# Performance work log

Measured on AMD Instinct MI355X. Metric: run time of the kernel, lower is better.

Reference implementation:

```python
import jax, jax.numpy as jnp
import numpy as np

N, E = 50000, 640000
DIN, DH, DOUT = 128, 256, 128


def _glorot(k, i, o):
    return jax.random.normal(k, (i, o), jnp.float32) / np.sqrt(i)


def setup_inputs() -> dict:
    key = jax.random.key(0)
    ks = jax.random.split(key, 12)
    return {
        "x": jax.random.normal(ks[0], (N, DIN), jnp.float32),
        "edge_index": jax.random.randint(ks[1], (2, E), 0, N, dtype=jnp.int32),
        # SAGEConv 1: in -> hidden (lin_l on aggregated w/ bias, lin_r on root)
        "W1l": _glorot(ks[2], DIN, DH), "b1l": jnp.zeros((DH,), jnp.float32), "W1r": _glorot(ks[3], DIN, DH),
        "g1": jnp.ones((DH,), jnp.float32), "be1": jnp.zeros((DH,), jnp.float32),
        # skip projection (in != hidden)
        "Wsk": _glorot(ks[4], DIN, DH), "bsk": jnp.zeros((DH,), jnp.float32),
        # SAGEConv 2: hidden -> hidden
        "W2l": _glorot(ks[5], DH, DH), "b2l": jnp.zeros((DH,), jnp.float32), "W2r": _glorot(ks[6], DH, DH),
        "g2": jnp.ones((DH,), jnp.float32), "be2": jnp.zeros((DH,), jnp.float32),
        # SAGEConv 3: hidden -> out
        "W3l": _glorot(ks[7], DH, DOUT), "b3l": jnp.zeros((DOUT,), jnp.float32), "W3r": _glorot(ks[8], DH, DOUT),
    }


def _sage_conv(x, src, dst, Wl, bl, Wr, n):
    # mean aggregation of source features into destination nodes
    msg = x[src]                                                 # [E, d]
    agg = jax.ops.segment_sum(msg, dst, num_segments=n)          # [N, d]
    cnt = jax.ops.segment_sum(jnp.ones((src.shape[0],), x.dtype), dst, num_segments=n)
    agg = agg / jnp.maximum(cnt, 1.0)[:, None]
    return agg @ Wl + bl + x @ Wr


def _layernorm(x, g, b):
    mu = jnp.mean(x, axis=-1, keepdims=True)
    var = jnp.mean((x - mu) ** 2, axis=-1, keepdims=True)
    return (x - mu) * jax.lax.rsqrt(var + 1e-5) * g + b


def reference(x, edge_index, W1l, b1l, W1r, g1, be1, Wsk, bsk,
              W2l, b2l, W2r, g2, be2, W3l, b3l, W3r):
    src, dst = edge_index[0], edge_index[1]
    n = x.shape[0]
    # layer 0: conv -> LN -> relu -> (dropout p=0, eval) -> skip via projection
    h = _sage_conv(x, src, dst, W1l, b1l, W1r, n)
    h = jax.nn.relu(_layernorm(h, g1, be1))
    h = h + (x @ Wsk + bsk)
    # layer 1: conv -> LN -> relu -> residual add (shapes match)
    h2 = _sage_conv(h, src, dst, W2l, b2l, W2r, n)
    h2 = jax.nn.relu(_layernorm(h2, g2, be2)) + h
    # final conv (no norm/act)
    return _sage_conv(h2, src, dst, W3l, b3l, W3r, n)
```

## Files before the change

kernel.cpp:

```cpp
#include <hip/hip_runtime.h>


typedef float floatx4 __attribute__((ext_vector_type(4)));
typedef float floatx2 __attribute__((ext_vector_type(2)));
typedef short bf16x8 __attribute__((ext_vector_type(8)));

__device__ inline unsigned short f2bf(float f) {
    unsigned u = __float_as_uint(f);
    unsigned r = (u + 0x7fffu + ((u >> 16) & 1u)) >> 16;
    return (unsigned short)r;
}
__device__ inline float bf2f_lo(unsigned v) { return __uint_as_float(v << 16); }
__device__ inline float bf2f_hi(unsigned v) { return __uint_as_float(v & 0xffff0000u); }

__device__ inline void gl_lds16(const void* g, void* l) {
    __builtin_amdgcn_global_load_lds((const __attribute__((address_space(1))) unsigned int*)g,
                                     (__attribute__((address_space(3))) unsigned int*)l,
                                     16, 0, 0);
}

__global__ void hist_kernel(const int* __restrict__ dst, int* __restrict__ cnt, int E) {
    int i = blockIdx.x * blockDim.x + threadIdx.x;
    if (i < E) atomicAdd(&cnt[dst[i]], 1);
}

#define SCAN_CHUNK 2048

__global__ __launch_bounds__(256) void scan_blocksums(const int* __restrict__ cnt,
                                                      int* __restrict__ bsum, int N) {
    __shared__ int sh[256];
    int t = threadIdx.x;
    int base = blockIdx.x * SCAN_CHUNK + t * 8;
    int s = 0;
#pragma unroll
    for (int i = 0; i < 8; i++) {
        int idx = base + i;
        if (idx < N) s += cnt[idx];
    }
    sh[t] = s;
    __syncthreads();
    for (int off = 1; off < 256; off <<= 1) {
        int v = (t >= off) ? sh[t - off] : 0;
        __syncthreads();
        sh[t] += v;
        __syncthreads();
    }
    if (t == 255) bsum[blockIdx.x] = sh[255];
}

__global__ __launch_bounds__(256) void scan_bsums(const int* __restrict__ bsum,
                                                  int* __restrict__ boff, int NB,
                                                  int* __restrict__ rowptr, int N, int E) {
    __shared__ int sh[256];
    int t = threadIdx.x;
    int v = (t < NB) ? bsum[t] : 0;
    sh[t] = v;
    __syncthreads();
    for (int off = 1; off < 256; off <<= 1) {
        int u = (t >= off) ? sh[t - off] : 0;
        __syncthreads();
        sh[t] += u;
        __syncthreads();
    }
    if (t < NB) boff[t] = sh[t] - v;
    if (t == 0) rowptr[N] = E;
}

__global__ __launch_bounds__(256) void scan_final(const int* __restrict__ cnt,
                                                  const int* __restrict__ boff,
                                                  int* __restrict__ rowptr,
                                                  int* __restrict__ cursor,
                                                  float* __restrict__ invdeg, int N) {
    __shared__ int sh[256];
    int t = threadIdx.x;
    int base = blockIdx.x * SCAN_CHUNK + t * 8;
    int c[8];
    int s = 0;
#pragma unroll
    for (int i = 0; i < 8; i++) {
        int idx = base + i;
        c[i] = (idx < N) ? cnt[idx] : 0;
        s += c[i];
    }
    sh[t] = s;
    __syncthreads();
    for (int off = 1; off < 256; off <<= 1) {
        int v = (t >= off) ? sh[t - off] : 0;
        __syncthreads();
        sh[t] += v;
        __syncthreads();
    }
    int run = boff[blockIdx.x] + sh[t] - s;
#pragma unroll
    for (int i = 0; i < 8; i++) {
        int idx = base + i;
        if (idx < N) {
            rowptr[idx] = run;
            cursor[idx] = run;
            invdeg[idx] = 1.0f / (float)(c[i] > 1 ? c[i] : 1);
            run += c[i];
        }
    }
}

__global__ void scatter_kernel(const int* __restrict__ src, const int* __restrict__ dst,
                               int* __restrict__ cursor, int* __restrict__ col, int E) {
    int i = blockIdx.x * blockDim.x + threadIdx.x;
    if (i < E) {
        int p = atomicAdd(&cursor[dst[i]], 1);
        col[p] = src[i];
    }
}

__global__ void prep_weights(const float* __restrict__ W1l, const float* __restrict__ W1r,
                             const float* __restrict__ Wsk, const float* __restrict__ W2l,
                             const float* __restrict__ W2r, const float* __restrict__ W3l,
                             const float* __restrict__ W3r, const float* __restrict__ b1l,
                             const float* __restrict__ bsk,
                             unsigned short* __restrict__ WtC, unsigned short* __restrict__ Wt2,
                             unsigned short* __restrict__ Wt3, float* __restrict__ biasC) {
    int i = blockIdx.x * blockDim.x + threadIdx.x;
    if (i < 32768) {
        int k = i >> 8, n = i & 255;
        WtC[n * 256 + k] = f2bf(W1l[i]);
    } else if (i < 65536) {
        int j = i - 32768, k = j >> 8, n = j & 255;
        WtC[n * 256 + 128 + k] = f2bf(W1r[j]);
    } else if (i < 98304) {
        int j = i - 65536, k = j >> 8, n = j & 255;
        WtC[(256 + n) * 256 + 128 + k] = f2bf(Wsk[j]);
    } else if (i < 131072) {
        int j = i - 98304, k = j >> 8, n = j & 255;
        WtC[(256 + n) * 256 + k] = 0;
    } else if (i < 196608) {
        int j = i - 131072, k = j >> 8, n = j & 255;
        Wt2[n * 512 + k] = f2bf(W2l[j]);
    } else if (i < 262144) {
        int j = i - 196608, k = j >> 8, n = j & 255;
        Wt2[n * 512 + 256 + k] = f2bf(W2r[j]);
    } else if (i < 294912) {
        int j = i - 262144, k = j >> 7, n = j & 127;
        Wt3[n * 256 + k] = f2bf(W3l[j]);
    } else if (i < 327680) {
        int j = i - 294912, k = j >> 7, n = j & 127;
        Wt3[(128 + n) * 256 + k] = f2bf(W3r[j]);
    } else if (i < 328192) {
        int j = i - 327680;
        biasC[j] = (j < 256) ? b1l[j] : bsk[j - 256];
    }
}

__global__ void cvt_x2(const float* __restrict__ x, unsigned short* __restrict__ A1cat,
                       unsigned char* __restrict__ X8, int total32) {
    int i = blockIdx.x * blockDim.x + threadIdx.x;
    if (i >= total32) return;
    int r = i >> 5, c4 = (i & 31) * 4;
    float4 v = *(const float4*)(x + (size_t)r * 128 + c4);
    ushort4 o;
    o.x = f2bf(v.x); o.y = f2bf(v.y); o.z = f2bf(v.z); o.w = f2bf(v.w);
    *(ushort4*)(A1cat + (size_t)r * 256 + 128 + c4) = o;
    unsigned wpk = 0;
    wpk = __builtin_amdgcn_cvt_pk_fp8_f32(v.x, v.y, wpk, false);
    wpk = __builtin_amdgcn_cvt_pk_fp8_f32(v.z, v.w, wpk, true);
    *(unsigned*)(X8 + (size_t)r * 128 + c4) = wpk;
}

__device__ inline void acc16_fp8(uint4 v, float m, floatx2* a) {
    floatx2 mm = {m, m};
    floatx2 p;
    p = __builtin_amdgcn_cvt_pk_f32_fp8(v.x, false); a[0] = p * mm + a[0];
    p = __builtin_amdgcn_cvt_pk_f32_fp8(v.x, true);  a[1] = p * mm + a[1];
    p = __builtin_amdgcn_cvt_pk_f32_fp8(v.y, false); a[2] = p * mm + a[2];
    p = __builtin_amdgcn_cvt_pk_f32_fp8(v.y, true);  a[3] = p * mm + a[3];
    p = __builtin_amdgcn_cvt_pk_f32_fp8(v.z, false); a[4] = p * mm + a[4];
    p = __builtin_amdgcn_cvt_pk_f32_fp8(v.z, true);  a[5] = p * mm + a[5];
    p = __builtin_amdgcn_cvt_pk_f32_fp8(v.w, false); a[6] = p * mm + a[6];
    p = __builtin_amdgcn_cvt_pk_f32_fp8(v.w, true);  a[7] = p * mm + a[7];
}

template <int RSB>
__global__ __launch_bounds__(256) void agg_fp8_g(const int* __restrict__ rowptr,
                                                 const int* __restrict__ col,
                                                 const float* __restrict__ invdeg,
                                                 const unsigned char* __restrict__ T8,
                                                 unsigned short* __restrict__ out, int ostride, int N) {
    constexpr int LPR = RSB / 16;
    constexpr int NPW = 64 / LPR;
    int wid = (blockIdx.x * blockDim.x + threadIdx.x) >> 6;
    int lane = threadIdx.x & 63;
    int sub = lane & (LPR - 1);
    int g = lane / LPR;
    int node = wid * NPW + g;
    bool vn = node < N;
    int nc = vn ? node : N - 1;
    int s = rowptr[nc];
    int e = vn ? rowptr[nc + 1] : s;
    const unsigned char* To = T8 + sub * 16;
    floatx2 a[8];
#pragma unroll
    for (int i = 0; i < 8; i++) a[i] = (floatx2){0.f, 0.f};
    for (int j = s; j < e; j += 4) {
        int j1 = (j + 1 < e) ? j + 1 : j;
        int j2 = (j + 2 < e) ? j + 2 : j;
        int j3 = (j + 3 < e) ? j + 3 : j;
        float m1 = (j + 1 < e) ? 1.f : 0.f;
        float m2 = (j + 2 < e) ? 1.f : 0.f;
        float m3 = (j + 3 < e) ? 1.f : 0.f;
        int c0 = col[j], c1 = col[j1], c2 = col[j2], c3 = col[j3];
        uint4 v0 = *(const uint4*)(To + (size_t)c0 * RSB);
        uint4 v1 = *(const uint4*)(To + (size_t)c1 * RSB);
        uint4 v2 = *(const uint4*)(To + (size_t)c2 * RSB);
        uint4 v3 = *(const uint4*)(To + (size_t)c3 * RSB);
        acc16_fp8(v0, 1.f, a);
        acc16_fp8(v1, m1, a);
        acc16_fp8(v2, m2, a);
        acc16_fp8(v3, m3, a);
    }
    if (vn) {
        float inv = invdeg[node];
        uint4 o1, o2;
        o1.x = (unsigned)f2bf(a[0].x * inv) | ((unsigned)f2bf(a[0].y * inv) << 16);
        o1.y = (unsigned)f2bf(a[1].x * inv) | ((unsigned)f2bf(a[1].y * inv) << 16);
        o1.z = (unsigned)f2bf(a[2].x * inv) | ((unsigned)f2bf(a[2].y * inv) << 16);
        o1.w = (unsigned)f2bf(a[3].x * inv) | ((unsigned)f2bf(a[3].y * inv) << 16);
        o2.x = (unsigned)f2bf(a[4].x * inv) | ((unsigned)f2bf(a[4].y * inv) << 16);
        o2.y = (unsigned)f2bf(a[5].x * inv) | ((unsigned)f2bf(a[5].y * inv) << 16);
        o2.z = (unsigned)f2bf(a[6].x * inv) | ((unsigned)f2bf(a[6].y * inv) << 16);
        o2.w = (unsigned)f2bf(a[7].x * inv) | ((unsigned)f2bf(a[7].y * inv) << 16);
        unsigned short* op = out + (size_t)node * ostride + sub * 16;
        *(uint4*)op = o1;
        *(uint4*)(op + 8) = o2;
    }
}

__global__ __launch_bounds__(256) void agg_fin_g(const int* __restrict__ rowptr,
                                                 const int* __restrict__ col,
                                                 const float* __restrict__ invdeg,
                                                 const unsigned short* __restrict__ T,
                                                 const float* __restrict__ R,
                                                 float* __restrict__ out, int N) {
    int wid = (blockIdx.x * blockDim.x + threadIdx.x) >> 6;
    int lane = threadIdx.x & 63;
    int sub = lane & 15;
    int g = lane >> 4;
    int node = wid * 4 + g;
    bool vn = node < N;
    int nc = vn ? node : N - 1;
    int s = rowptr[nc];
    int e = vn ? rowptr[nc + 1] : s;
    const unsigned short* To = T + sub * 8;
    floatx2 a[4];
#pragma unroll
    for (int i = 0; i < 4; i++) a[i] = (floatx2){0.f, 0.f};
    for (int j = s; j < e; j += 4) {
        int j1 = (j + 1 < e) ? j + 1 : j;
        int j2 = (j + 2 < e) ? j + 2 : j;
        int j3 = (j + 3 < e) ? j + 3 : j;
        float m1 = (j + 1 < e) ? 1.f : 0.f;
        float m2 = (j + 2 < e) ? 1.f : 0.f;
        float m3 = (j + 3 < e) ? 1.f : 0.f;
        int c0 = col[j], c1 = col[j1], c2 = col[j2], c3 = col[j3];
        uint4 v0 = *(const uint4*)(To + (size_t)c0 * 128);
        uint4 v1 = *(const uint4*)(To + (size_t)c1 * 128);
        uint4 v2 = *(const uint4*)(To + (size_t)c2 * 128);
        uint4 v3 = *(const uint4*)(To + (size_t)c3 * 128);
        floatx2 mm;
        floatx2 p;
        mm = (floatx2){1.f, 1.f};
        p = (floatx2){bf2f_lo(v0.x), bf2f_hi(v0.x)}; a[0] = p + a[0];
        p = (floatx2){bf2f_lo(v0.y), bf2f_hi(v0.y)}; a[1] = p + a[1];
        p = (floatx2){bf2f_lo(v0.z), bf2f_hi(v0.z)}; a[2] = p + a[2];
        p = (floatx2){bf2f_lo(v0.w), bf2f_hi(v0.w)}; a[3] = p + a[3];
        mm = (floatx2){m1, m1};
        p = (floatx2){bf2f_lo(v1.x), bf2f_hi(v1.x)}; a[0] = p * mm + a[0];
        p = (floatx2){bf2f_lo(v1.y), bf2f_hi(v1.y)}; a[1] = p * mm + a[1];
        p = (floatx2){bf2f_lo(v1.z), bf2f_hi(v1.z)}; a[2] = p * mm + a[2];
        p = (floatx2){bf2f_lo(v1.w), bf2f_hi(v1.w)}; a[3] = p * mm + a[3];
        mm = (floatx2){m2, m2};
        p = (floatx2){bf2f_lo(v2.x), bf2f_hi(v2.x)}; a[0] = p * mm + a[0];
        p = (floatx2){bf2f_lo(v2.y), bf2f_hi(v2.y)}; a[1] = p * mm + a[1];
        p = (floatx2){bf2f_lo(v2.z), bf2f_hi(v2.z)}; a[2] = p * mm + a[2];
        p = (floatx2){bf2f_lo(v2.w), bf2f_hi(v2.w)}; a[3] = p * mm + a[3];
        mm = (floatx2){m3, m3};
        p = (floatx2){bf2f_lo(v3.x), bf2f_hi(v3.x)}; a[0] = p * mm + a[0];
        p = (floatx2){bf2f_lo(v3.y), bf2f_hi(v3.y)}; a[1] = p * mm + a[1];
        p = (floatx2){bf2f_lo(v3.z), bf2f_hi(v3.z)}; a[2] = p * mm + a[2];
        p = (floatx2){bf2f_lo(v3.w), bf2f_hi(v3.w)}; a[3] = p * mm + a[3];
    }
    if (vn) {
        float inv = invdeg[node];
        const float* Rp = R + (size_t)node * 128 + sub * 8;
        float4 r1 = *(const float4*)Rp;
        float4 r2 = *(const float4*)(Rp + 4);
        float4 o1, o2;
        o1.x = a[0].x * inv + r1.x; o1.y = a[0].y * inv + r1.y;
        o1.z = a[1].x * inv + r1.z; o1.w = a[1].y * inv + r1.w;
        o2.x = a[2].x * inv + r2.x; o2.y = a[2].y * inv + r2.y;
        o2.z = a[3].x * inv + r2.z; o2.w = a[3].y * inv + r2.w;
        float* op = out + (size_t)node * 128 + sub * 8;
        *(float4*)op = o1;
        *(float4*)(op + 4) = o2;
    }
}

template <int KIT, int NPAN, int MODE>
__global__ __launch_bounds__(512) void gemm_fused(
    const unsigned short* __restrict__ A, int lda,
    const unsigned short* __restrict__ B, int ldb,
    const float* __restrict__ bias,
    const float* __restrict__ gamma, const float* __restrict__ beta,
    const unsigned short* __restrict__ resid,
    unsigned short* __restrict__ outb,
    unsigned char* __restrict__ h8,
    float* __restrict__ outf, int M) {
    constexpr int COLS = NPAN * 256;
    constexpr int LNW = COLS + 8;
    constexpr int STAGE_E = 128 * 64;
    constexpr int STAGE_F = 2 * STAGE_E / 2;
    constexpr int SMEM_F = (STAGE_F > 32 * LNW) ? STAGE_F : 32 * LNW;
    __shared__ __align__(16) float smemf[SMEM_F];
    unsigned short* sbase = (unsigned short*)smemf;

    int t = threadIdx.x;
    int lane = t & 63, w = t >> 6;
    int bm = blockIdx.x * 128;
    int wm = (w & 1) * 64, wn = (w >> 1) * 64;
    int m16 = lane & 15, kq = lane >> 4;

    floatx4 acc[NPAN][4][4];
#pragma unroll
    for (int p = 0; p < NPAN; p++)
#pragma unroll
        for (int i = 0; i < 4; i++)
#pragma unroll
            for (int j = 0; j < 4; j++) acc[p][i][j] = (floatx4){0.f, 0.f, 0.f, 0.f};

    const int s_row0 = t >> 3;
    const int s_j = t & 7;

    auto stage = [&](int kt, int bsel) {
        unsigned short* s = sbase + bsel * STAGE_E;
        int k0 = kt * 64;
#pragma unroll
        for (int i = 0; i < 2; i++) {
            int row = s_row0 + i * 64;
            int kc = s_j ^ (row & 7);
            int rowA = bm + row;
            if (rowA > M - 1) rowA = M - 1;
            gl_lds16(A + (size_t)rowA * lda + k0 + kc * 8, (void*)&s[(size_t)(i * 512 + t) * 8]);
        }
    };

    stage(0, 0);
    __syncthreads();
    for (int kt = 0; kt < KIT; kt++) {
        if (kt + 1 < KIT) stage(kt + 1, (kt & 1) ^ 1);
        const unsigned short* sA = sbase + (kt & 1) * STAGE_E;
#pragma unroll
        for (int ks = 0; ks < 2; ks++) {
            int kcl = (ks << 2) | kq;
            bf16x8 af[4];
#pragma unroll
            for (int mi = 0; mi < 4; mi++)
                af[mi] = *(const bf16x8*)&sA[(wm + mi * 16 + m16) * 64 + (kcl ^ (m16 & 7)) * 8];
#pragma unroll
            for (int p = 0; p < NPAN; p++) {
                if (MODE == 0 && p == 1 && kt * 64 < 128) continue;
                const unsigned short* Bp = B + (size_t)(wn + p * 256) * ldb + kt * 64;
                bf16x8 bf[4];
#pragma unroll
                for (int ni = 0; ni < 4; ni++)
                    bf[ni] = *(const bf16x8*)&Bp[(size_t)(ni * 16 + m16) * ldb + kcl * 8];
#pragma unroll
                for (int mi = 0; mi < 4; mi++)
#pragma unroll
                    for (int ni = 0; ni < 4; ni++)
                        acc[p][mi][ni] =
                            __builtin_amdgcn_mfma_f32_16x16x32_bf16(af[mi], bf[ni], acc[p][mi][ni], 0, 0, 0);
            }
        }
        __syncthreads();
    }

    float* lnb = smemf;
    int c4 = lane * 4;
    float4 bu = {0.f, 0.f, 0.f, 0.f}, bs = {0.f, 0.f, 0.f, 0.f};
    float4 gv = {0.f, 0.f, 0.f, 0.f}, bv = {0.f, 0.f, 0.f, 0.f};
    float4 b3 = {0.f, 0.f, 0.f, 0.f};
    if (MODE == 0) {
        bu = *(const float4*)&bias[c4];
        bs = *(const float4*)&bias[256 + c4];
        gv = *(const float4*)&gamma[c4];
        bv = *(const float4*)&beta[c4];
    } else if (MODE == 1) {
        bu = *(const float4*)&bias[c4];
        gv = *(const float4*)&gamma[c4];
        bv = *(const float4*)&beta[c4];
    } else {
        if (lane >= 32) b3 = *(const float4*)&bias[c4 - 128];
    }

#pragma unroll
    for (int g4 = 0; g4 < 4; g4++) {
        if (wm == (g4 >> 1) * 64) {
            int mi0 = (g4 & 1) * 2;
#pragma unroll
            for (int p = 0; p < NPAN; p++)
#pragma unroll
                for (int mm = 0; mm < 2; mm++)
#pragma unroll
                    for (int ni = 0; ni < 4; ni++)
#pragma unroll
                        for (int r = 0; r < 4; r++)
                            lnb[(mm * 16 + kq * 4 + r) * LNW + wn + p * 256 + ni * 16 + m16] =
                                acc[p][mi0 + mm][ni][r];
        }
        __syncthreads();
#pragma unroll
        for (int rr = 0; rr < 4; rr++) {
            int lrow = w * 4 + rr;
            int grow = bm + g4 * 32 + lrow;
            bool valid = grow < M;
            float4 u = *(const float4*)&lnb[lrow * LNW + c4];
            if (MODE <= 1) {
                u.x += bu.x; u.y += bu.y; u.z += bu.z; u.w += bu.w;
                float s1 = (u.x + u.y) + (u.z + u.w);
                float s2 = (u.x * u.x + u.y * u.y) + (u.z * u.z + u.w * u.w);
#pragma unroll
                for (int off = 1; off < 64; off <<= 1) {
                    s1 += __shfl_xor(s1, off, 64);
                    s2 += __shfl_xor(s2, off, 64);
                }
                float mu = s1 * (1.f / 256.f);
                float var = s2 * (1.f / 256.f) - mu * mu;
                float rs = rsqrtf(var + 1e-5f);
                float a0, a1, a2, a3;
                if (MODE == 0) {
                    float4 sv = *(const float4*)&lnb[lrow * LNW + 256 + c4];
                    a0 = sv.x + bs.x; a1 = sv.y + bs.y; a2 = sv.z + bs.z; a3 = sv.w + bs.w;
                } else {
                    int gr = valid ? grow : M - 1;
                    uint2 hv = *(const uint2*)(resid + (size_t)gr * 512 + c4);
                    a0 = bf2f_lo(hv.x); a1 = bf2f_hi(hv.x); a2 = bf2f_lo(hv.y); a3 = bf2f_hi(hv.y);
                }
                float o0 = fmaxf((u.x - mu) * rs * gv.x + bv.x, 0.f) + a0;
                float o1 = fmaxf((u.y - mu) * rs * gv.y + bv.y, 0.f) + a1;
                float o2 = fmaxf((u.z - mu) * rs * gv.z + bv.z, 0.f) + a2;
                float o3 = fmaxf((u.w - mu) * rs * gv.w + bv.w, 0.f) + a3;
                if (valid) {
                    ushort4 o;
                    o.x = f2bf(o0); o.y = f2bf(o1); o.z = f2bf(o2); o.w = f2bf(o3);
                    *(ushort4*)(outb + (size_t)grow * 512 + c4) = o;
                    if (MODE == 0) {
                        unsigned wpk = 0;
                        wpk = __builtin_amdgcn_cvt_pk_fp8_f32(o0, o1, wpk, false);
                        wpk = __builtin_amdgcn_cvt_pk_fp8_f32(o2, o3, wpk, true);
                        *(unsigned*)(h8 + (size_t)grow * 256 + c4) = wpk;
                    }
                }
            } else {
                if (valid) {
                    if (lane < 32) {
                        ushort4 o;
                        o.x = f2bf(u.x); o.y = f2bf(u.y); o.z = f2bf(u.z); o.w = f2bf(u.w);
                        *(ushort4*)(outb + (size_t)grow * 128 + c4) = o;
                    } else {
                        float4 o;
                        o.x = u.x + b3.x; o.y = u.y + b3.y; o.z = u.z + b3.z; o.w = u.w + b3.w;
                        *(float4*)(outf + (size_t)grow * 128 + (c4 - 128)) = o;
                    }
                }
            }
        }
        __syncthreads();
    }
}

extern "C" void kernel_launch(void* const* d_in, const int* in_sizes, int n_in,
                              void* d_out, int out_size, void* d_ws, size_t ws_size,
                              hipStream_t stream) {
    const float* x   = (const float*)d_in[0];
    const int*   ei  = (const int*)d_in[1];
    const float* W1l = (const float*)d_in[2];
    const float* b1l = (const float*)d_in[3];
    const float* W1r = (const float*)d_in[4];
    const float* g1  = (const float*)d_in[5];
    const float* be1 = (const float*)d_in[6];
    const float* Wsk = (const float*)d_in[7];
    const float* bsk = (const float*)d_in[8];
    const float* W2l = (const float*)d_in[9];
    const float* b2l = (const float*)d_in[10];
    const float* W2r = (const float*)d_in[11];
    const float* g2  = (const float*)d_in[12];
    const float* be2 = (const float*)d_in[13];
    const float* W3l = (const float*)d_in[14];
    const float* b3l = (const float*)d_in[15];
    const float* W3r = (const float*)d_in[16];

    const int N = in_sizes[0] / 128;
    const int E = in_sizes[1] / 2;
    const int* src = ei;
    const int* dst = ei + E;

    char* p = (char*)d_ws;
    auto alloc = [&](size_t bytes) {
        void* r = (void*)p;
        p += (bytes + 255) & ~(size_t)255;
        return r;
    };
    int*   cnt    = (int*)alloc(sizeof(int) * N);
    int*   rowptr = (int*)alloc(sizeof(int) * (N + 1));
    int*   cursor = (int*)alloc(sizeof(int) * N);
    float* invdeg = (float*)alloc(sizeof(float) * N);
    int*   col    = (int*)alloc(sizeof(int) * E);
    int*   bsum   = (int*)alloc(sizeof(int) * 256);
    int*   boff   = (int*)alloc(sizeof(int) * 256);
    unsigned short* A1cat = (unsigned short*)alloc(sizeof(short) * (size_t)N * 256);
    unsigned short* A2cat = (unsigned short*)alloc(sizeof(short) * (size_t)N * 512);
    float* r3 = (float*)alloc(sizeof(float) * (size_t)N * 128);
    unsigned char* H8 = (unsigned char*)alloc((size_t)N * 256);
    unsigned char* X8 = (unsigned char*)alloc((size_t)N * 128);
    unsigned short* WtC = (unsigned short*)alloc(sizeof(short) * 512 * 256);
    unsigned short* Wt2 = (unsigned short*)alloc(sizeof(short) * 256 * 512);
    unsigned short* Wt3 = (unsigned short*)alloc(sizeof(short) * 256 * 256);
    float* biasC = (float*)alloc(sizeof(float) * 512);
    unsigned short* t3 = A1cat;

    hipMemsetAsync(cnt, 0, sizeof(int) * N, stream);
    hist_kernel<<<(E + 255) / 256, 256, 0, stream>>>(dst, cnt, E);
    int NB = (N + SCAN_CHUNK - 1) / SCAN_CHUNK;
    scan_blocksums<<<NB, 256, 0, stream>>>(cnt, bsum, N);
    scan_bsums<<<1, 256, 0, stream>>>(bsum, boff, NB, rowptr, N, E);
    scan_final<<<NB, 256, 0, stream>>>(cnt, boff, rowptr, cursor, invdeg, N);
    scatter_kernel<<<(E + 255) / 256, 256, 0, stream>>>(src, dst, cursor, col, E);

    prep_weights<<<(328192 + 255) / 256, 256, 0, stream>>>(W1l, W1r, Wsk, W2l, W2r, W3l, W3r,
                                                           b1l, bsk, WtC, Wt2, Wt3, biasC);
    cvt_x2<<<((N * 32) + 255) / 256, 256, 0, stream>>>(x, A1cat, X8, N * 32);

    int mBlocks = (N + 127) / 128;
    int agg1Blocks = (N + 31) / 32;
    int agg2Blocks = (N + 15) / 16;
    int aggFBlocks = (N + 15) / 16;

    agg_fp8_g<128><<<agg1Blocks, 256, 0, stream>>>(rowptr, col, invdeg, X8, A1cat, 256, N);
    gemm_fused<4, 2, 0><<<mBlocks, 512, 0, stream>>>(A1cat, 256, WtC, 256, biasC, g1, be1,
                                                     nullptr, A2cat + 256, H8, nullptr, N);

    agg_fp8_g<256><<<agg2Blocks, 256, 0, stream>>>(rowptr, col, invdeg, H8, A2cat, 512, N);
    gemm_fused<8, 1, 1><<<mBlocks, 512, 0, stream>>>(A2cat, 512, Wt2, 512, b2l, g2, be2,
                                                     A2cat + 256, A2cat, nullptr, nullptr, N);

    gemm_fused<4, 1, 2><<<mBlocks, 512, 0, stream>>>(A2cat, 512, Wt3, 256, b3l, nullptr, nullptr,
                                                     nullptr, t3, nullptr, r3, N);
    agg_fin_g<<<aggFBlocks, 256, 0, stream>>>(rowptr, col, invdeg, t3, r3, (float*)d_out, N);
}
```

Baseline: 376.9 us.

## Fuse layer-2 GEMM+LayerNorm with layer-3 GEMM, keeping h2 in LDS

Layer 2's GEMM with LayerNorm, ReLU and residual is merged with layer 3's dual projection GEMM in one kernel. The bf16 h2 tile is written into shared memory in the swizzled A layout and used directly as the A operand for the second GEMM. This removes one launch plus the global write and re-read of h2. In exchange, shared memory per block grows to about 64KB plus the LayerNorm buffer, which may lower occupancy. The layer-1 GEMM is split out into its own non-templated kernel.

```diff
diff --git a/kernel.cpp b/kernel.cpp
--- a/kernel.cpp
+++ b/kernel.cpp
@@ -266,7 +266,6 @@
         uint4 v3 = *(const uint4*)(To + (size_t)c3 * 128);
         floatx2 mm;
         floatx2 p;
-        mm = (floatx2){1.f, 1.f};
         p = (floatx2){bf2f_lo(v0.x), bf2f_hi(v0.x)}; a[0] = p + a[0];
         p = (floatx2){bf2f_lo(v0.y), bf2f_hi(v0.y)}; a[1] = p + a[1];
         p = (floatx2){bf2f_lo(v0.z), bf2f_hi(v0.z)}; a[2] = p + a[2];
@@ -303,16 +302,15 @@
     }
 }
 
-template <int KIT, int NPAN, int MODE>
-__global__ __launch_bounds__(512) void gemm_fused(
+__global__ __launch_bounds__(512) void gemm_l1(
     const unsigned short* __restrict__ A, int lda,
     const unsigned short* __restrict__ B, int ldb,
     const float* __restrict__ bias,
     const float* __restrict__ gamma, const float* __restrict__ beta,
-    const unsigned short* __restrict__ resid,
     unsigned short* __restrict__ outb,
-    unsigned char* __restrict__ h8,
-    float* __restrict__ outf, int M) {
+    unsigned char* __restrict__ h8, int M) {
+    constexpr int KIT = 4;
+    constexpr int NPAN = 2;
     constexpr int COLS = NPAN * 256;
     constexpr int LNW = COLS + 8;
     constexpr int STAGE_E = 128 * 64;
@@ -326,6 +324,7 @@
     int bm = blockIdx.x * 128;
     int wm = (w & 1) * 64, wn = (w >> 1) * 64;
     int m16 = lane & 15, kq = lane >> 4;
+    const int fsw = m16 & 7;
 
     floatx4 acc[NPAN][4][4];
 #pragma unroll
@@ -337,7 +336,6 @@
 
     const int s_row0 = t >> 3;
     const int s_j = t & 7;
-
     auto stage = [&](int kt, int bsel) {
         unsigned short* s = sbase + bsel * STAGE_E;
         int k0 = kt * 64;
@@ -362,10 +360,10 @@
             bf16x8 af[4];
 #pragma unroll
             for (int mi = 0; mi < 4; mi++)
-                af[mi] = *(const bf16x8*)&sA[(wm + mi * 16 + m16) * 64 + (kcl ^ (m16 & 7)) * 8];
+                af[mi] = *(const bf16x8*)&sA[(wm + mi * 16 + m16) * 64 + (kcl ^ fsw) * 8];
 #pragma unroll
             for (int p = 0; p < NPAN; p++) {
-                if (MODE == 0 && p == 1 && kt * 64 < 128) continue;
+                if (p == 1 && kt * 64 < 128) continue;
                 const unsigned short* Bp = B + (size_t)(wn + p * 256) * ldb + kt * 64;
                 bf16x8 bf[4];
 #pragma unroll
@@ -384,21 +382,10 @@
 
     float* lnb = smemf;
     int c4 = lane * 4;
-    float4 bu = {0.f, 0.f, 0.f, 0.f}, bs = {0.f, 0.f, 0.f, 0.f};
-    float4 gv = {0.f, 0.f, 0.f, 0.f}, bv = {0.f, 0.f, 0.f, 0.f};
-    float4 b3 = {0.f, 0.f, 0.f, 0.f};
-    if (MODE == 0) {
-        bu = *(const float4*)&bias[c4];
-        bs = *(const float4*)&bias[256 + c4];
-        gv = *(const float4*)&gamma[c4];
-        bv = *(const float4*)&beta[c4];
-    } else if (MODE == 1) {
-        bu = *(const float4*)&bias[c4];
-        gv = *(const float4*)&gamma[c4];
-        bv = *(const float4*)&beta[c4];
-    } else {
-        if (lane >= 32) b3 = *(const float4*)&bias[c4 - 128];
-    }
+    float4 bu = *(const float4*)&bias[c4];
+    float4 bs = *(const float4*)&bias[256 + c4];
+    float4 gv = *(const float4*)&gamma[c4];
+    float4 bv = *(const float4*)&beta[c4];
 
 #pragma unroll
     for (int g4 = 0; g4 < 4; g4++) {
@@ -422,53 +409,225 @@
             int grow = bm + g4 * 32 + lrow;
             bool valid = grow < M;
             float4 u = *(const float4*)&lnb[lrow * LNW + c4];
-            if (MODE <= 1) {
-                u.x += bu.x; u.y += bu.y; u.z += bu.z; u.w += bu.w;
-                float s1 = (u.x + u.y) + (u.z + u.w);
-                float s2 = (u.x * u.x + u.y * u.y) + (u.z * u.z + u.w * u.w);
-#pragma unroll
-                for (int off = 1; off < 64; off <<= 1) {
-                    s1 += __shfl_xor(s1, off, 64);
-                    s2 += __shfl_xor(s2, off, 64);
-                }
-                float mu = s1 * (1.f / 256.f);
-                float var = s2 * (1.f / 256.f) - mu * mu;
-                float rs = rsqrtf(var + 1e-5f);
-                float a0, a1, a2, a3;
-                if (MODE == 0) {
-                    float4 sv = *(const float4*)&lnb[lrow * LNW + 256 + c4];
-                    a0 = sv.x + bs.x; a1 = sv.y + bs.y; a2 = sv.z + bs.z; a3 = sv.w + bs.w;
+            u.x += bu.x; u.y += bu.y; u.z += bu.z; u.w += bu.w;
+            float s1 = (u.x + u.y) + (u.z + u.w);
+            float s2 = (u.x * u.x + u.y * u.y) + (u.z * u.z + u.w * u.w);
+#pragma unroll
+            for (int off = 1; off < 64; off <<= 1) {
+                s1 += __shfl_xor(s1, off, 64);
+                s2 += __shfl_xor(s2, off, 64);
+            }
+            float mu = s1 * (1.f / 256.f);
+            float var = s2 * (1.f / 256.f) - mu * mu;
+            float rs = rsqrtf(var + 1e-5f);
+            float4 sv = *(const float4*)&lnb[lrow * LNW + 256 + c4];
+            float a0 = sv.x + bs.x, a1 = sv.y + bs.y, a2 = sv.z + bs.z, a3 = sv.w + bs.w;
+            float o0 = fmaxf((u.x - mu) * rs * gv.x + bv.x, 0.f) + a0;
+            float o1 = fmaxf((u.y - mu) * rs * gv.y + bv.y, 0.f) + a1;
+            float o2 = fmaxf((u.z - mu) * rs * gv.z + bv.z, 0.f) + a2;
+            float o3 = fmaxf((u.w - mu) * rs * gv.w + bv.w, 0.f) + a3;
+            if (valid) {
+                ushort4 o;
+                o.x = f2bf(o0); o.y = f2bf(o1); o.z = f2bf(o2); o.w = f2bf(o3);
+                *(ushort4*)(outb + (size_t)grow * 512 + c4) = o;
+                unsigned wpk = 0;
+                wpk = __builtin_amdgcn_cvt_pk_fp8_f32(o0, o1, wpk, false);
+                wpk = __builtin_amdgcn_cvt_pk_fp8_f32(o2, o3, wpk, true);
+                *(unsigned*)(h8 + (size_t)grow * 256 + c4) = wpk;
+            }
+        }
+        __syncthreads();
+    }
+}
+
+__global__ __launch_bounds__(512) void gemm23_fused(
+    const unsigned short* __restrict__ A,
+    const unsigned short* __restrict__ B2,
+    const float* __restrict__ b2,
+    const float* __restrict__ g2v, const float* __restrict__ be2v,
+    const unsigned short* __restrict__ resid,
+    const unsigned short* __restrict__ B3,
+    const float* __restrict__ b3,
+    unsigned short* __restrict__ t3,
+    float* __restrict__ r3, int M) {
+    constexpr int KIT = 8;
+    constexpr int LNW = 256 + 8;
+    constexpr int STAGE_E = 128 * 64;
+    __shared__ __align__(16) char smem[65536 + 32 * LNW * 4];
+    unsigned short* Ab = (unsigned short*)smem;
+    float* lnb = (float*)(smem + 65536);
+
+    int t = threadIdx.x;
+    int lane = t & 63, w = t >> 6;
+    int bm = blockIdx.x * 128;
+    int wm = (w & 1) * 64, wn = (w >> 1) * 64;
+    int m16 = lane & 15, kq = lane >> 4;
+    const int fsw = m16 & 7;
+
+    floatx4 acc[4][4];
+#pragma unroll
+    for (int i = 0; i < 4; i++)
+#pragma unroll
+        for (int j = 0; j < 4; j++) acc[i][j] = (floatx4){0.f, 0.f, 0.f, 0.f};
+
+    const int s_row0 = t >> 3;
+    const int s_j = t & 7;
+    auto stage = [&](int kt, int bsel) {
+        unsigned short* s = Ab + bsel * STAGE_E;
+        int k0 = kt * 64;
+#pragma unroll
+        for (int i = 0; i < 2; i++) {
+            int row = s_row0 + i * 64;
+            int kc = s_j ^ (row & 7);
+            int rowA = bm + row;
+            if (rowA > M - 1) rowA = M - 1;
+            gl_lds16(A + (size_t)rowA * 512 + k0 + kc * 8, (void*)&s[(size_t)(i * 512 + t) * 8]);
+        }
+    };
+
+    stage(0, 0);
+    __syncthreads();
+    for (int kt = 0; kt < KIT; kt++) {
+        if (kt + 1 < KIT) stage(kt + 1, (kt & 1) ^ 1);
+        const unsigned short* sA = Ab + (kt & 1) * STAGE_E;
+#pragma unroll
+        for (int ks = 0; ks < 2; ks++) {
+            int kcl = (ks << 2) | kq;
+            bf16x8 af[4];
+#pragma unroll
+            for (int mi = 0; mi < 4; mi++)
+                af[mi] = *(const bf16x8*)&sA[(wm + mi * 16 + m16) * 64 + (kcl ^ fsw) * 8];
+            const unsigned short* Bp = B2 + (size_t)wn * 512 + kt * 64;
+            bf16x8 bf[4];
+#pragma unroll
+            for (int ni = 0; ni < 4; ni++)
+                bf[ni] = *(const bf16x8*)&Bp[(size_t)(ni * 16 + m16) * 512 + kcl * 8];
+#pragma unroll
+            for (int mi = 0; mi < 4; mi++)
+#pragma unroll
+                for (int ni = 0; ni < 4; ni++)
+                    acc[mi][ni] =
+                        __builtin_amdgcn_mfma_f32_16x16x32_bf16(af[mi], bf[ni], acc[mi][ni], 0, 0, 0);
+        }
+        __syncthreads();
+    }
+
+    int c4 = lane * 4;
+    float4 bu = *(const float4*)&b2[c4];
+    float4 gv = *(const float4*)&g2v[c4];
+    float4 bv = *(const float4*)&be2v[c4];
+    const int a_kt = lane >> 4;
+    const int a_ch = (lane >> 1) & 7;
+    const int a_wi = (lane & 1) * 4;
+#pragma unroll
+    for (int g4 = 0; g4 < 4; g4++) {
+        if (wm == (g4 >> 1) * 64) {
+            int mi0 = (g4 & 1) * 2;
+#pragma unroll
+            for (int mm = 0; mm < 2; mm++)
+#pragma unroll
+                for (int ni = 0; ni < 4; ni++)
+#pragma unroll
+                    for (int r = 0; r < 4; r++)
+                        lnb[(mm * 16 + kq * 4 + r) * LNW + wn + ni * 16 + m16] =
+                            acc[mi0 + mm][ni][r];
+        }
+        __syncthreads();
+#pragma unroll
+        for (int rr = 0; rr < 4; rr++) {
+            int lrow = w * 4 + rr;
+            int grow = bm + g4 * 32 + lrow;
+            bool valid = grow < M;
+            float4 u = *(const float4*)&lnb[lrow * LNW + c4];
+            u.x += bu.x; u.y += bu.y; u.z += bu.z; u.w += bu.w;
+            float s1 = (u.x + u.y) + (u.z + u.w);
+            float s2 = (u.x * u.x + u.y * u.y) + (u.z * u.z + u.w * u.w);
+#pragma unroll
+            for (int off = 1; off < 64; off <<= 1) {
+                s1 += __shfl_xor(s1, off, 64);
+                s2 += __shfl_xor(s2, off, 64);
+            }
+            float mu = s1 * (1.f / 256.f);
+            float var = s2 * (1.f / 256.f) - mu * mu;
+            float rs = rsqrtf(var + 1e-5f);
+            int gr = valid ? grow : M - 1;
+            uint2 hv = *(const uint2*)(resid + (size_t)gr * 512 + c4);
+            float a0 = bf2f_lo(hv.x), a1 = bf2f_hi(hv.x), a2 = bf2f_lo(hv.y), a3 = bf2f_hi(hv.y);
+            float o0 = fmaxf((u.x - mu) * rs * gv.x + bv.x, 0.f) + a0;
+            float o1 = fmaxf((u.y - mu) * rs * gv.y + bv.y, 0.f) + a1;
+            float o2 = fmaxf((u.z - mu) * rs * gv.z + bv.z, 0.f) + a2;
+            float o3 = fmaxf((u.w - mu) * rs * gv.w + bv.w, 0.f) + a3;
+            int row = g4 * 32 + lrow;
+            uint2 h2p;
+            h2p.x = (unsigned)f2bf(o0) | ((unsigned)f2bf(o1) << 16);
+            h2p.y = (unsigned)f2bf(o2) | ((unsigned)f2bf(o3) << 16);
+            *(uint2*)&Ab[(size_t)a_kt * 8192 + (size_t)row * 64 +
+                         (size_t)((a_ch ^ (row & 7)) * 8 + a_wi)] = h2p;
+        }
+        __syncthreads();
+    }
+
+    floatx4 acc2[4][4];
+#pragma unroll
+    for (int i = 0; i < 4; i++)
+#pragma unroll
+        for (int j = 0; j < 4; j++) acc2[i][j] = (floatx4){0.f, 0.f, 0.f, 0.f};
+#pragma unroll
+    for (int kt = 0; kt < 4; kt++) {
+        const unsigned short* sT = Ab + kt * 8192;
+#pragma unroll
+        for (int ks = 0; ks < 2; ks++) {
+            int kcl = (ks << 2) | kq;
+            bf16x8 af[4];
+#pragma unroll
+            for (int mi = 0; mi < 4; mi++)
+                af[mi] = *(const bf16x8*)&sT[(wm + mi * 16 + m16) * 64 + (kcl ^ fsw) * 8];
+            const unsigned short* Bp = B3 + (size_t)wn * 256 + kt * 64;
+            bf16x8 bf[4];
+#pragma unroll
+            for (int ni = 0; ni < 4; ni++)
+                bf[ni] = *(const bf16x8*)&Bp[(size_t)(ni * 16 + m16) * 256 + kcl * 8];
+#pragma unroll
+            for (int mi = 0; mi < 4; mi++)
+#pragma unroll
+                for (int ni = 0; ni < 4; ni++)
+                    acc2[mi][ni] =
+                        __builtin_amdgcn_mfma_f32_16x16x32_bf16(af[mi], bf[ni], acc2[mi][ni], 0, 0, 0);
+        }
+    }
+    __syncthreads();
+
+    float4 b3v = {0.f, 0.f, 0.f, 0.f};
+    if (lane >= 32) b3v = *(const float4*)&b3[c4 - 128];
+#pragma unroll
+    for (int g4 = 0; g4 < 4; g4++) {
+        if (wm == (g4 >> 1) * 64) {
+            int mi0 = (g4 & 1) * 2;
+#pragma unroll
+            for (int mm = 0; mm < 2; mm++)
+#pragma unroll
+                for (int ni = 0; ni < 4; ni++)
+#pragma unroll
+                    for (int r = 0; r < 4; r++)
+                        lnb[(mm * 16 + kq * 4 + r) * LNW + wn + ni * 16 + m16] =
+                            acc2[mi0 + mm][ni][r];
+        }
+        __syncthreads();
+#pragma unroll
+        for (int rr = 0; rr < 4; rr++) {
+            int lrow = w * 4 + rr;
+            int grow = bm + g4 * 32 + lrow;
+            bool valid = grow < M;
+            float4 u = *(const float4*)&lnb[lrow * LNW + c4];
+            if (valid) {
+                if (lane < 32) {
+                    ushort4 o;
+                    o.x = f2bf(u.x); o.y = f2bf(u.y); o.z = f2bf(u.z); o.w = f2bf(u.w);
+                    *(ushort4*)(t3 + (size_t)grow * 128 + c4) = o;
                 } else {
-                    int gr = valid ? grow : M - 1;
-                    uint2 hv = *(const uint2*)(resid + (size_t)gr * 512 + c4);
-                    a0 = bf2f_lo(hv.x); a1 = bf2f_hi(hv.x); a2 = bf2f_lo(hv.y); a3 = bf2f_hi(hv.y);
-                }
-                float o0 = fmaxf((u.x - mu) * rs * gv.x + bv.x, 0.f) + a0;
-                float o1 = fmaxf((u.y - mu) * rs * gv.y + bv.y, 0.f) + a1;
-                float o2 = fmaxf((u.z - mu) * rs * gv.z + bv.z, 0.f) + a2;
-                float o3 = fmaxf((u.w - mu) * rs * gv.w + bv.w, 0.f) + a3;
-                if (valid) {
-                    ushort4 o;
-                    o.x = f2bf(o0); o.y = f2bf(o1); o.z = f2bf(o2); o.w = f2bf(o3);
-                    *(ushort4*)(outb + (size_t)grow * 512 + c4) = o;
-                    if (MODE == 0) {
-                        unsigned wpk = 0;
-                        wpk = __builtin_amdgcn_cvt_pk_fp8_f32(o0, o1, wpk, false);
-                        wpk = __builtin_amdgcn_cvt_pk_fp8_f32(o2, o3, wpk, true);
-                        *(unsigned*)(h8 + (size_t)grow * 256 + c4) = wpk;
-                    }
-                }
-            } else {
-                if (valid) {
-                    if (lane < 32) {
-                        ushort4 o;
-                        o.x = f2bf(u.x); o.y = f2bf(u.y); o.z = f2bf(u.z); o.w = f2bf(u.w);
-                        *(ushort4*)(outb + (size_t)grow * 128 + c4) = o;
-                    } else {
-                        float4 o;
-                        o.x = u.x + b3.x; o.y = u.y + b3.y; o.z = u.z + b3.z; o.w = u.w + b3.w;
-                        *(float4*)(outf + (size_t)grow * 128 + (c4 - 128)) = o;
-                    }
+                    float4 o;
+                    o.x = u.x + b3v.x; o.y = u.y + b3v.y; o.z = u.z + b3v.z; o.w = u.w + b3v.w;
+                    *(float4*)(r3 + (size_t)grow * 128 + (c4 - 128)) = o;
                 }
             }
         }
@@ -544,14 +703,12 @@
     int aggFBlocks = (N + 15) / 16;
 
     agg_fp8_g<128><<<agg1Blocks, 256, 0, stream>>>(rowptr, col, invdeg, X8, A1cat, 256, N);
-    gemm_fused<4, 2, 0><<<mBlocks, 512, 0, stream>>>(A1cat, 256, WtC, 256, biasC, g1, be1,
-                                                     nullptr, A2cat + 256, H8, nullptr, N);
+    gemm_l1<<<mBlocks, 512, 0, stream>>>(A1cat, 256, WtC, 256, biasC, g1, be1,
+                                         A2cat + 256, H8, N);
 
     agg_fp8_g<256><<<agg2Blocks, 256, 0, stream>>>(rowptr, col, invdeg, H8, A2cat, 512, N);
-    gemm_fused<8, 1, 1><<<mBlocks, 512, 0, stream>>>(A2cat, 512, Wt2, 512, b2l, g2, be2,
-                                                     A2cat + 256, A2cat, nullptr, nullptr, N);
-
-    gemm_fused<4, 1, 2><<<mBlocks, 512, 0, stream>>>(A2cat, 512, Wt3, 256, b3l, nullptr, nullptr,
-                                                     nullptr, t3, nullptr, r3, N);
+    gemm23_fused<<<mBlocks, 512, 0, stream>>>(A2cat, Wt2, b2l, g2, be2, A2cat + 256,
+                                              Wt3, b3l, t3, r3, N);
+
     agg_fin_g<<<aggFBlocks, 256, 0, stream>>>(rowptr, col, invdeg, t3, r3, (float*)d_out, N);
 }
```

After: 382.5 us. No clear change (+1.5%).
